# Kernel tuning notes

Measured on AMD Instinct MI355X. Metric: run time of the kernel, lower is better.

Reference implementation:

```python
import jax, jax.numpy as jnp
import numpy as np

D = 32       # input_dim (dims[0])
PREV = 64    # dims[-2], bottleneck prev_dim
HID = 128    # dims[-1], bottleneck hidden dim
HDIM = 64    # hypernet hidden dim
NW = (D + 1) * PREV  # 2112 generated weights for the single net1 layer
BATCH = 8192


def setup_inputs() -> dict:
    key = jax.random.key(0)
    ks = jax.random.split(key, 10)
    s = 0.1  # keep tanh in its active range
    return {
        "y": jax.random.normal(ks[0], (BATCH, D + 1), dtype=jnp.float32),
        "t": jax.random.uniform(ks[1], (1,), dtype=jnp.float32),
        "hw1": jax.random.normal(ks[2], (HDIM, 1), dtype=jnp.float32) * s,
        "hb1": jax.random.normal(ks[3], (HDIM,), dtype=jnp.float32) * s,
        "hw2": jax.random.normal(ks[4], (NW, HDIM), dtype=jnp.float32) * s,
        "hb2": jax.random.normal(ks[5], (NW,), dtype=jnp.float32) * s,
        "bw": jax.random.normal(ks[6], (HID, PREV), dtype=jnp.float32) * s,
        "bb": jax.random.normal(ks[7], (HID,), dtype=jnp.float32) * s,
        "w2": jax.random.normal(ks[8], (D, HID), dtype=jnp.float32) * s,
        "b2": jax.random.normal(ks[9], (D,), dtype=jnp.float32) * s,
    }


def reference(y, t, hw1, hb1, hw2, hb2, bw, bb, w2, b2):
    x = y[:, :-1]                       # (B, D): drop logdet channel
    B = x.shape[0]

    # Hypernet: Linear(1,HDIM) -> tanh -> Linear(HDIM, NW), input is t as (1,1)
    hcode = jnp.tanh(t.reshape(1, 1) @ hw1.T + hb1)      # (1, HDIM)
    weights = (hcode @ hw2.T + hb2).reshape(-1)          # (NW,)
    w1 = weights[: D * PREV].reshape(D, PREV)            # (D, PREV)
    b1 = weights[D * PREV:].reshape(1, PREV)             # (1, PREV)

    # net1: single layer of HypernetMLP([D, PREV]) -> affine, no activation
    def net1(Ytile):
        return Ytile @ w1 + b1          # (HID, B, PREV)

    Y = jnp.broadcast_to(x[None], (HID, B, D))           # expanded copies
    H, vjp_net1 = jax.vjp(net1, Y)                       # H: (HID, B, PREV)

    # CNFBottleneck: per-hidden-unit dot product + tanh
    s = jnp.einsum('hbp,hp->hb', H, bw) + bb[:, None]    # (HID, B)
    a = jnp.tanh(s)                                      # elem_outputs[...,0]

    # d/dH of sum(a): closed-form tanh derivative times bottleneck row
    elem_grad = (1.0 - a * a)[:, :, None] * bw[:, None, :]   # (HID, B, PREV)

    h_out = a.T                                          # (B, HID)
    dx = h_out @ w2.T + b2                               # (B, D)

    # Backprop elem_grad through net1 to get dH/dY contribution per hidden unit
    grad_inputs, = vjp_net1(elem_grad)                   # (HID, B, D)

    # divergence = sum_h <grad_inputs[h,b,:], w2.T[h,:]>
    div = jnp.einsum('hbd,hd->b', grad_inputs, w2.T)     # (B,)

    return jnp.concatenate([dx, -div[:, None]], axis=1)  # (B, D+1)
```

## Files before the change

kernel.cpp:

```cpp
#include <hip/hip_runtime.h>
#include <math.h>

#define D    32
#define PREV 64
#define HID  128
#define HDIM 64
#define BPB  32


__global__ __launch_bounds__(128) void prep_kernel(
    const float* __restrict__ t,
    const float* __restrict__ hw1,
    const float* __restrict__ hb1,
    const float* __restrict__ hw2,
    const float* __restrict__ hb2,
    const float* __restrict__ bw,
    const float* __restrict__ bb,
    const float* __restrict__ w2,
    float* __restrict__ ws)
{
    __shared__ float hcode[HDIM];
    __shared__ float w1s[2][64];
    __shared__ float b1s[PREV];

    const int tid = threadIdx.x;
    const int blk = blockIdx.x;

    if (tid < HDIM) hcode[tid] = tanhf(t[0] * hw1[tid] + hb1[tid]);
    __syncthreads();

    if (blk < 16) {
        const int i = blk * 128 + tid;
        {
            const float4* row = reinterpret_cast<const float4*>(hw2 + (size_t)i * HDIM);
            float acc = hb2[i];
            #pragma unroll
            for (int q = 0; q < 16; ++q) {
                float4 u = row[q];
                int j = q * 4;
                acc += u.x * hcode[j] + u.y * hcode[j + 1]
                     + u.z * hcode[j + 2] + u.w * hcode[j + 3];
            }
            w1s[tid >> 6][tid & 63] = acc;
        }
        __syncthreads();

        for (int idx = tid; idx < 256; idx += 128) {
            const int h = idx & 127, dd = idx >> 7;
            const int d = 2 * blk + dd;
            const float4* bwr = reinterpret_cast<const float4*>(bw + h * PREV);
            const float* w1r = &w1s[dd][0];
            float acc = 0.f;
            #pragma unroll
            for (int q = 0; q < 16; ++q) {
                float4 u = bwr[q];
                int p = q * 4;
                acc += u.x * w1r[p]     + u.y * w1r[p + 1]
                     + u.z * w1r[p + 2] + u.w * w1r[p + 3];
            }
            ws[h * D + d] = acc;
            ws[8192 + h * D + d] = w2[d * HID + h];
        }
    } else {
        if (tid < PREV) {
            const int i = 2048 + tid;
            const float4* row = reinterpret_cast<const float4*>(hw2 + (size_t)i * HDIM);
            float acc = hb2[i];
            #pragma unroll
            for (int q = 0; q < 16; ++q) {
                float4 u = row[q];
                int j = q * 4;
                acc += u.x * hcode[j] + u.y * hcode[j + 1]
                     + u.z * hcode[j + 2] + u.w * hcode[j + 3];
            }
            b1s[tid] = acc;
        }
        __syncthreads();
        {
            const float4* bwr = reinterpret_cast<const float4*>(bw + tid * PREV);
            float acc = bb[tid];
            #pragma unroll
            for (int q = 0; q < 16; ++q) {
                float4 u = bwr[q];
                int p = q * 4;
                acc += u.x * b1s[p]     + u.y * b1s[p + 1]
                     + u.z * b1s[p + 2] + u.w * b1s[p + 3];
            }
            ws[4096 + tid] = acc;
        }
    }
}

__global__ __launch_bounds__(128) void main_kernel(
    const float* __restrict__ y,
    const float* __restrict__ ws,
    const float* __restrict__ b2,
    float* __restrict__ out)
{
    __shared__ float Ms[HID][36];
    __shared__ float Ws[HID][36];
    __shared__ float xs[BPB][36];
    __shared__ __align__(16) float os[BPB][33];
    __shared__ float sbias_s[HID];
    __shared__ float cs_s[HID];
    __shared__ float b2s[D];

    const int tid = threadIdx.x;
    const int blk = blockIdx.x;

    {
        const float4* m4 = reinterpret_cast<const float4*>(ws);
        const float4* w4 = reinterpret_cast<const float4*>(ws + 8192);
        #pragma unroll
        for (int it = 0; it < 8; ++it) {
            int i = it * 128 + tid;
            int h = i >> 3;
            int dq = (i & 7) << 2;
            *reinterpret_cast<float4*>(&Ms[h][dq]) = m4[i];
            *reinterpret_cast<float4*>(&Ws[h][dq]) = w4[i];
        }
    }
    {
        const float4* yb4 = reinterpret_cast<const float4*>(y + (size_t)blk * BPB * 33);
        for (int i = tid; i < 264; i += 128) {
            float4 v = yb4[i];
            int base = 4 * i;
            int r0 = base / 33, c0 = base - 33 * r0;
            float vv[4] = { v.x, v.y, v.z, v.w };
            #pragma unroll
            for (int j = 0; j < 4; ++j) {
                int c = c0 + j, r = r0;
                if (c >= 33) { c -= 33; r += 1; }
                xs[r][c] = vv[j];
            }
        }
    }
    sbias_s[tid] = ws[4096 + tid];
    if (tid < D) b2s[tid] = b2[tid];
    __syncthreads();

    {
        const float4* mr = reinterpret_cast<const float4*>(&Ms[tid][0]);
        const float4* wr = reinterpret_cast<const float4*>(&Ws[tid][0]);
        float acc = 0.f;
        #pragma unroll
        for (int q = 0; q < 8; ++q) {
            float4 m = mr[q], w = wr[q];
            acc += m.x * w.x + m.y * w.y + m.z * w.z + m.w * w.w;
        }
        cs_s[tid] = acc;
    }
    __syncthreads();

    const int bsub2 = tid >> 3;
    const int hg    = tid & 7;
    const int b0 = 2 * bsub2, b1 = b0 + 1;

    float xr0[D], xr1[D];
    {
        const float4* x0 = reinterpret_cast<const float4*>(&xs[b0][0]);
        const float4* x1 = reinterpret_cast<const float4*>(&xs[b1][0]);
        #pragma unroll
        for (int q = 0; q < 8; ++q) {
            float4 v0 = x0[q], v1 = x1[q];
            xr0[4*q] = v0.x; xr0[4*q+1] = v0.y; xr0[4*q+2] = v0.z; xr0[4*q+3] = v0.w;
            xr1[4*q] = v1.x; xr1[4*q+1] = v1.y; xr1[4*q+2] = v1.z; xr1[4*q+3] = v1.w;
        }
    }

    float dx0[D], dx1[D];
    #pragma unroll
    for (int d = 0; d < D; ++d) { dx0[d] = 0.f; dx1[d] = 0.f; }
    float div0 = 0.f, div1 = 0.f;

    #pragma unroll
    for (int k = 0; k < 16; ++k) {
        const int h = (k << 3) | hg;
        float s0 = sbias_s[h], s1 = s0;
        const float4* mrow = reinterpret_cast<const float4*>(&Ms[h][0]);
        #pragma unroll
        for (int q = 0; q < 8; ++q) {
            float4 m = mrow[q];
            s0 += xr0[4*q]*m.x + xr0[4*q+1]*m.y + xr0[4*q+2]*m.z + xr0[4*q+3]*m.w;
            s1 += xr1[4*q]*m.x + xr1[4*q+1]*m.y + xr1[4*q+2]*m.z + xr1[4*q+3]*m.w;
        }
        float e0 = __expf(2.f * s0), e1 = __expf(2.f * s1);
        float a0 = 1.f - 2.f / (e0 + 1.f);
        float a1 = 1.f - 2.f / (e1 + 1.f);
        float ch = cs_s[h];
        div0 += (1.f - a0 * a0) * ch;
        div1 += (1.f - a1 * a1) * ch;
        const float4* wrow = reinterpret_cast<const float4*>(&Ws[h][0]);
        #pragma unroll
        for (int q = 0; q < 8; ++q) {
            float4 w = wrow[q];
            dx0[4*q]   += a0 * w.x;  dx1[4*q]   += a1 * w.x;
            dx0[4*q+1] += a0 * w.y;  dx1[4*q+1] += a1 * w.y;
            dx0[4*q+2] += a0 * w.z;  dx1[4*q+2] += a1 * w.z;
            dx0[4*q+3] += a0 * w.w;  dx1[4*q+3] += a1 * w.w;
        }
    }

    #pragma unroll
    for (int m = 1; m < 8; m <<= 1) {
        #pragma unroll
        for (int d = 0; d < D; ++d) {
            dx0[d] += __shfl_xor(dx0[d], m, 64);
            dx1[d] += __shfl_xor(dx1[d], m, 64);
        }
        div0 += __shfl_xor(div0, m, 64);
        div1 += __shfl_xor(div1, m, 64);
    }

    if (hg == 0) {
        #pragma unroll
        for (int d = 0; d < D; ++d) {
            os[b0][d] = dx0[d] + b2s[d];
            os[b1][d] = dx1[d] + b2s[d];
        }
        os[b0][D] = -div0;
        os[b1][D] = -div1;
    }
    __syncthreads();

    {
        const float4* os4 = reinterpret_cast<const float4*>(&os[0][0]);
        float4* ob4 = reinterpret_cast<float4*>(out + (size_t)blk * BPB * 33);
        for (int i = tid; i < 264; i += 128)
            ob4[i] = os4[i];
    }
}

extern "C" void kernel_launch(void* const* d_in, const int* in_sizes, int n_in,
                              void* d_out, int out_size, void* d_ws, size_t ws_size,
                              hipStream_t stream) {
    const float* y   = (const float*)d_in[0];
    const float* t   = (const float*)d_in[1];
    const float* hw1 = (const float*)d_in[2];
    const float* hb1 = (const float*)d_in[3];
    const float* hw2 = (const float*)d_in[4];
    const float* hb2 = (const float*)d_in[5];
    const float* bw  = (const float*)d_in[6];
    const float* bb  = (const float*)d_in[7];
    const float* w2  = (const float*)d_in[8];
    const float* b2  = (const float*)d_in[9];
    float* ws  = (float*)d_ws;
    float* out = (float*)d_out;

    hipLaunchKernelGGL(prep_kernel, dim3(17), dim3(128), 0, stream,
                       t, hw1, hb1, hw2, hb2, bw, bb, w2, ws);
    hipLaunchKernelGGL(main_kernel, dim3(8192 / BPB), dim3(128), 0, stream,
                       y, ws, b2, out);
}
```

Measured before the change: 87.59 us.

## Spread hidden units over 32 lanes, halve batch per block, reduce with DPP

Each block now handles 16 batch rows with 256 threads, so 512 blocks are launched instead of 256. Each group of 32 lanes covers one pair of rows, and each lane processes 4 hidden units instead of 16. The cross-lane reduction of the dx and div partials now uses DPP row operations (quad xor, row rotate, row broadcast15) instead of a shuffle butterfly over 8 lanes. This shortens the serial per-thread loop and makes the reduction cheaper, but every block reloads the 32 KB of Ms/Ws weights, so total shared-memory fill traffic doubles and the reduction now spans 32 lanes instead of 8.

```diff
diff --git a/kernel.cpp b/kernel.cpp
--- a/kernel.cpp
+++ b/kernel.cpp
@@ -5,8 +5,30 @@
 #define PREV 64
 #define HID  128
 #define HDIM 64
-#define BPB  32
-
+#define BPB  16
+#define TPB  256
+
+
+#define DPP_QUAD_XOR1   0xB1
+#define DPP_QUAD_XOR2   0x4E
+#define DPP_ROW_ROR4    0x124
+#define DPP_ROW_ROR8    0x128
+#define DPP_ROW_BCAST15 0x142
+
+template <int CTRL>
+__device__ __forceinline__ float dpp_radd(float v) {
+    int t = __builtin_amdgcn_update_dpp(0, __float_as_int(v), CTRL, 0xF, 0xF, true);
+    return v + __int_as_float(t);
+}
+
+__device__ __forceinline__ float reduce32(float v) {
+    v = dpp_radd<DPP_QUAD_XOR1>(v);
+    v = dpp_radd<DPP_QUAD_XOR2>(v);
+    v = dpp_radd<DPP_ROW_ROR4>(v);
+    v = dpp_radd<DPP_ROW_ROR8>(v);
+    v = dpp_radd<DPP_ROW_BCAST15>(v);
+    return v;
+}
 
 __global__ __launch_bounds__(128) void prep_kernel(
     const float* __restrict__ t,
@@ -91,7 +113,7 @@
     }
 }
 
-__global__ __launch_bounds__(128) void main_kernel(
+__global__ __launch_bounds__(TPB) void main_kernel(
     const float* __restrict__ y,
     const float* __restrict__ ws,
     const float* __restrict__ b2,
@@ -112,8 +134,8 @@
         const float4* m4 = reinterpret_cast<const float4*>(ws);
         const float4* w4 = reinterpret_cast<const float4*>(ws + 8192);
         #pragma unroll
-        for (int it = 0; it < 8; ++it) {
-            int i = it * 128 + tid;
+        for (int it = 0; it < 4; ++it) {
+            int i = it * TPB + tid;
             int h = i >> 3;
             int dq = (i & 7) << 2;
             *reinterpret_cast<float4*>(&Ms[h][dq]) = m4[i];
@@ -122,9 +144,9 @@
     }
     {
         const float4* yb4 = reinterpret_cast<const float4*>(y + (size_t)blk * BPB * 33);
-        for (int i = tid; i < 264; i += 128) {
-            float4 v = yb4[i];
-            int base = 4 * i;
+        if (tid < 132) {
+            float4 v = yb4[tid];
+            int base = 4 * tid;
             int r0 = base / 33, c0 = base - 33 * r0;
             float vv[4] = { v.x, v.y, v.z, v.w };
             #pragma unroll
@@ -135,11 +157,11 @@
             }
         }
     }
-    sbias_s[tid] = ws[4096 + tid];
-    if (tid < D) b2s[tid] = b2[tid];
-    __syncthreads();
-
-    {
+    if (tid < HID) sbias_s[tid] = ws[4096 + tid];
+    if (tid < D)   b2s[tid] = b2[tid];
+    __syncthreads();
+
+    if (tid < HID) {
         const float4* mr = reinterpret_cast<const float4*>(&Ms[tid][0]);
         const float4* wr = reinterpret_cast<const float4*>(&Ws[tid][0]);
         float acc = 0.f;
@@ -150,11 +172,10 @@
         }
         cs_s[tid] = acc;
     }
-    __syncthreads();
-
-    const int bsub2 = tid >> 3;
-    const int hg    = tid & 7;
-    const int b0 = 2 * bsub2, b1 = b0 + 1;
+
+    const int hg   = tid & 31;
+    const int pair = tid >> 5;
+    const int b0 = 2 * pair, b1 = b0 + 1;
 
     float xr0[D], xr1[D];
     {
@@ -167,6 +188,7 @@
             xr1[4*q] = v1.x; xr1[4*q+1] = v1.y; xr1[4*q+2] = v1.z; xr1[4*q+3] = v1.w;
         }
     }
+    __syncthreads();
 
     float dx0[D], dx1[D];
     #pragma unroll
@@ -174,8 +196,8 @@
     float div0 = 0.f, div1 = 0.f;
 
     #pragma unroll
-    for (int k = 0; k < 16; ++k) {
-        const int h = (k << 3) | hg;
+    for (int k = 0; k < 4; ++k) {
+        const int h = (k << 5) | hg;
         float s0 = sbias_s[h], s1 = s0;
         const float4* mrow = reinterpret_cast<const float4*>(&Ms[h][0]);
         #pragma unroll
@@ -202,17 +224,14 @@
     }
 
     #pragma unroll
-    for (int m = 1; m < 8; m <<= 1) {
-        #pragma unroll
-        for (int d = 0; d < D; ++d) {
-            dx0[d] += __shfl_xor(dx0[d], m, 64);
-            dx1[d] += __shfl_xor(dx1[d], m, 64);
-        }
-        div0 += __shfl_xor(div0, m, 64);
-        div1 += __shfl_xor(div1, m, 64);
-    }
-
-    if (hg == 0) {
+    for (int d = 0; d < D; ++d) {
+        dx0[d] = reduce32(dx0[d]);
+        dx1[d] = reduce32(dx1[d]);
+    }
+    div0 = reduce32(div0);
+    div1 = reduce32(div1);
+
+    if (hg == 16) {
         #pragma unroll
         for (int d = 0; d < D; ++d) {
             os[b0][d] = dx0[d] + b2s[d];
@@ -226,8 +245,7 @@
     {
         const float4* os4 = reinterpret_cast<const float4*>(&os[0][0]);
         float4* ob4 = reinterpret_cast<float4*>(out + (size_t)blk * BPB * 33);
-        for (int i = tid; i < 264; i += 128)
-            ob4[i] = os4[i];
+        if (tid < 132) ob4[tid] = os4[tid];
     }
 }
 
@@ -249,6 +267,6 @@
 
     hipLaunchKernelGGL(prep_kernel, dim3(17), dim3(128), 0, stream,
                        t, hw1, hb1, hw2, hb2, bw, bb, w2, ws);
-    hipLaunchKernelGGL(main_kernel, dim3(8192 / BPB), dim3(128), 0, stream,
+    hipLaunchKernelGGL(main_kernel, dim3(8192 / BPB), dim3(TPB), 0, stream,
                        y, ws, b2, out);
 }
```

Result: faster. 84.23 us (-3.8%).

## Map batch rows to lanes and split hidden units across waves

Applied to the files above, without the earlier changes.

Restructures the main kernel so each lane owns one batch row and each of 8 waves handles 16 hidden units. The M/W matrices are read from global memory with wave-uniform addresses (scalar loads) instead of being staged in LDS. Partial dx/div results are reduced through a shared-memory buffer instead of cross-lane shuffles. Blocks grow to 512 threads covering 64 rows, halving grid size to 128 blocks, which may underfill the GPU. The change also adds a dynamic LDS buffer of about 67KB.

```diff
diff --git a/kernel.cpp b/kernel.cpp
--- a/kernel.cpp
+++ b/kernel.cpp
@@ -5,7 +5,11 @@
 #define PREV 64
 #define HID  128
 #define HDIM 64
-#define BPB  32
+
+#define MB_BATCH   64
+#define MB_THREADS 512
+#define NWAVE      8
+#define HPW        (HID / NWAVE)
 
 
 __global__ __launch_bounds__(128) void prep_kernel(
@@ -91,16 +95,14 @@
     }
 }
 
-__global__ __launch_bounds__(128) void main_kernel(
+__global__ __launch_bounds__(MB_THREADS) void main_kernel(
     const float* __restrict__ y,
     const float* __restrict__ ws,
     const float* __restrict__ b2,
     float* __restrict__ out)
 {
-    __shared__ float Ms[HID][36];
-    __shared__ float Ws[HID][36];
-    __shared__ float xs[BPB][36];
-    __shared__ __align__(16) float os[BPB][33];
+    extern __shared__ float buf[];
+    __shared__ float xs[MB_BATCH][36];
     __shared__ float sbias_s[HID];
     __shared__ float cs_s[HID];
     __shared__ float b2s[D];
@@ -109,20 +111,8 @@
     const int blk = blockIdx.x;
 
     {
-        const float4* m4 = reinterpret_cast<const float4*>(ws);
-        const float4* w4 = reinterpret_cast<const float4*>(ws + 8192);
-        #pragma unroll
-        for (int it = 0; it < 8; ++it) {
-            int i = it * 128 + tid;
-            int h = i >> 3;
-            int dq = (i & 7) << 2;
-            *reinterpret_cast<float4*>(&Ms[h][dq]) = m4[i];
-            *reinterpret_cast<float4*>(&Ws[h][dq]) = w4[i];
-        }
-    }
-    {
-        const float4* yb4 = reinterpret_cast<const float4*>(y + (size_t)blk * BPB * 33);
-        for (int i = tid; i < 264; i += 128) {
+        const float4* yb4 = reinterpret_cast<const float4*>(y + (size_t)blk * MB_BATCH * 33);
+        for (int i = tid; i < 528; i += MB_THREADS) {
             float4 v = yb4[i];
             int base = 4 * i;
             int r0 = base / 33, c0 = base - 33 * r0;
@@ -135,13 +125,9 @@
             }
         }
     }
-    sbias_s[tid] = ws[4096 + tid];
-    if (tid < D) b2s[tid] = b2[tid];
-    __syncthreads();
-
-    {
-        const float4* mr = reinterpret_cast<const float4*>(&Ms[tid][0]);
-        const float4* wr = reinterpret_cast<const float4*>(&Ws[tid][0]);
+    if (tid < HID) {
+        const float4* mr = reinterpret_cast<const float4*>(ws + tid * D);
+        const float4* wr = reinterpret_cast<const float4*>(ws + 8192 + tid * D);
         float acc = 0.f;
         #pragma unroll
         for (int q = 0; q < 8; ++q) {
@@ -149,85 +135,73 @@
             acc += m.x * w.x + m.y * w.y + m.z * w.z + m.w * w.w;
         }
         cs_s[tid] = acc;
+    } else if (tid < 2 * HID) {
+        sbias_s[tid - HID] = ws[4096 + (tid - HID)];
+    } else if (tid < 2 * HID + D) {
+        b2s[tid - 2 * HID] = b2[tid - 2 * HID];
     }
     __syncthreads();
 
-    const int bsub2 = tid >> 3;
-    const int hg    = tid & 7;
-    const int b0 = 2 * bsub2, b1 = b0 + 1;
-
-    float xr0[D], xr1[D];
-    {
-        const float4* x0 = reinterpret_cast<const float4*>(&xs[b0][0]);
-        const float4* x1 = reinterpret_cast<const float4*>(&xs[b1][0]);
+    const int lane = tid & 63;
+    const int wid  = __builtin_amdgcn_readfirstlane(tid >> 6);
+    const int h0   = wid * HPW;
+
+    float x[D];
+    {
+        const float4* xr = reinterpret_cast<const float4*>(&xs[lane][0]);
         #pragma unroll
         for (int q = 0; q < 8; ++q) {
-            float4 v0 = x0[q], v1 = x1[q];
-            xr0[4*q] = v0.x; xr0[4*q+1] = v0.y; xr0[4*q+2] = v0.z; xr0[4*q+3] = v0.w;
-            xr1[4*q] = v1.x; xr1[4*q+1] = v1.y; xr1[4*q+2] = v1.z; xr1[4*q+3] = v1.w;
-        }
-    }
-
-    float dx0[D], dx1[D];
+            float4 v = xr[q];
+            x[4*q] = v.x; x[4*q+1] = v.y; x[4*q+2] = v.z; x[4*q+3] = v.w;
+        }
+    }
+
+    float dx[D];
     #pragma unroll
-    for (int d = 0; d < D; ++d) { dx0[d] = 0.f; dx1[d] = 0.f; }
-    float div0 = 0.f, div1 = 0.f;
+    for (int d = 0; d < D; ++d) dx[d] = 0.f;
+    float dv = 0.f;
 
     #pragma unroll
-    for (int k = 0; k < 16; ++k) {
-        const int h = (k << 3) | hg;
-        float s0 = sbias_s[h], s1 = s0;
-        const float4* mrow = reinterpret_cast<const float4*>(&Ms[h][0]);
-        #pragma unroll
-        for (int q = 0; q < 8; ++q) {
-            float4 m = mrow[q];
-            s0 += xr0[4*q]*m.x + xr0[4*q+1]*m.y + xr0[4*q+2]*m.z + xr0[4*q+3]*m.w;
-            s1 += xr1[4*q]*m.x + xr1[4*q+1]*m.y + xr1[4*q+2]*m.z + xr1[4*q+3]*m.w;
-        }
-        float e0 = __expf(2.f * s0), e1 = __expf(2.f * s1);
-        float a0 = 1.f - 2.f / (e0 + 1.f);
-        float a1 = 1.f - 2.f / (e1 + 1.f);
-        float ch = cs_s[h];
-        div0 += (1.f - a0 * a0) * ch;
-        div1 += (1.f - a1 * a1) * ch;
-        const float4* wrow = reinterpret_cast<const float4*>(&Ws[h][0]);
-        #pragma unroll
-        for (int q = 0; q < 8; ++q) {
-            float4 w = wrow[q];
-            dx0[4*q]   += a0 * w.x;  dx1[4*q]   += a1 * w.x;
-            dx0[4*q+1] += a0 * w.y;  dx1[4*q+1] += a1 * w.y;
-            dx0[4*q+2] += a0 * w.z;  dx1[4*q+2] += a1 * w.z;
-            dx0[4*q+3] += a0 * w.w;  dx1[4*q+3] += a1 * w.w;
-        }
-    }
-
-    #pragma unroll
-    for (int m = 1; m < 8; m <<= 1) {
-        #pragma unroll
-        for (int d = 0; d < D; ++d) {
-            dx0[d] += __shfl_xor(dx0[d], m, 64);
-            dx1[d] += __shfl_xor(dx1[d], m, 64);
-        }
-        div0 += __shfl_xor(div0, m, 64);
-        div1 += __shfl_xor(div1, m, 64);
-    }
-
-    if (hg == 0) {
-        #pragma unroll
-        for (int d = 0; d < D; ++d) {
-            os[b0][d] = dx0[d] + b2s[d];
-            os[b1][d] = dx1[d] + b2s[d];
-        }
-        os[b0][D] = -div0;
-        os[b1][D] = -div1;
+    for (int hi = 0; hi < HPW; ++hi) {
+        const int h = h0 + hi;
+        const float* __restrict__ Mr = ws + h * D;
+        const float* __restrict__ Wr = ws + 8192 + h * D;
+        float p0 = 0.f, p1 = 0.f, p2 = 0.f, p3 = 0.f;
+        #pragma unroll
+        for (int d = 0; d < D; d += 4) {
+            p0 += Mr[d]     * x[d];
+            p1 += Mr[d + 1] * x[d + 1];
+            p2 += Mr[d + 2] * x[d + 2];
+            p3 += Mr[d + 3] * x[d + 3];
+        }
+        float s = sbias_s[h] + ((p0 + p1) + (p2 + p3));
+        float e = __expf(2.f * s);
+        float a = 1.f - 2.f / (e + 1.f);
+        dv += (1.f - a * a) * cs_s[h];
+        #pragma unroll
+        for (int d = 0; d < D; ++d)
+            dx[d] += a * Wr[d];
+    }
+
+    {
+        float* my = buf + ((size_t)(wid * MB_BATCH) + lane) * 33;
+        #pragma unroll
+        for (int d = 0; d < D; ++d) my[d] = dx[d];
+        my[D] = dv;
     }
     __syncthreads();
 
     {
-        const float4* os4 = reinterpret_cast<const float4*>(&os[0][0]);
-        float4* ob4 = reinterpret_cast<float4*>(out + (size_t)blk * BPB * 33);
-        for (int i = tid; i < 264; i += 128)
-            ob4[i] = os4[i];
+        float* ob = out + (size_t)blk * MB_BATCH * 33;
+        for (int i = tid; i < MB_BATCH * 33; i += MB_THREADS) {
+            float r = 0.f;
+            #pragma unroll
+            for (int w = 0; w < NWAVE; ++w)
+                r += buf[w * (MB_BATCH * 33) + i];
+            int c = i % 33;
+            r = (c < 32) ? (r + b2s[c]) : -r;
+            ob[i] = r;
+        }
     }
 }
 
@@ -249,6 +223,7 @@
 
     hipLaunchKernelGGL(prep_kernel, dim3(17), dim3(128), 0, stream,
                        t, hw1, hb1, hw2, hb2, bw, bb, w2, ws);
-    hipLaunchKernelGGL(main_kernel, dim3(8192 / BPB), dim3(128), 0, stream,
+    hipLaunchKernelGGL(main_kernel, dim3(8192 / MB_BATCH), dim3(MB_THREADS),
+                       NWAVE * MB_BATCH * 33 * sizeof(float), stream,
                        y, ws, b2, out);
 }
```

Measured after the change: 86.03 us. Within noise of the previous version (-1.8%).
